# Kernel tuning notes

Measured on AMD Instinct MI355X. Metric: run time of the kernel, lower is better.

## Reference

```python
import jax, jax.numpy as jnp
import numpy as np


def setup_inputs() -> dict:
    key = jax.random.key(0)
    k1, k2 = jax.random.split(key)
    B, C, P, D, K = 8, 8, 512, 256, 8192
    z = jax.random.normal(k1, (B, C, P, D), dtype=jnp.float32)
    # codebook initialized with std = 1/sqrt(dim), matching nn.init.normal_
    codebook = jax.random.normal(k2, (K, D), dtype=jnp.float32) / np.sqrt(D).astype(np.float32)
    return {"z": z, "codebook": codebook}


def reference(z, codebook):
    B, C, P, D = z.shape
    z_flat = z.reshape(-1, D)  # [N, D]
    # squared-L2 distances: ||z||^2 - 2 z.cb^T + ||cb||^2  -> [N, K]
    dist = (
        jnp.sum(z_flat * z_flat, axis=1, keepdims=True)
        - 2.0 * jnp.matmul(z_flat, codebook.T)
        + jnp.sum(codebook * codebook, axis=1)[None, :]
    )
    codes = jnp.argmin(dist, axis=1)  # [N]
    z_q = codebook[codes].reshape(B, C, P, D)
    commit_loss = 0.25 * jnp.mean((jax.lax.stop_gradient(z_q) - z) ** 2)
    codebook_loss = jnp.mean((z_q - jax.lax.stop_gradient(z)) ** 2)
    total_loss = commit_loss + 0.25 * codebook_loss
    # straight-through estimator
    z_q_st = z + jax.lax.stop_gradient(z_q - z)
    return (z_q_st, total_loss, codes)
```

## Files before the change

### kernel.cpp

```cpp
#include <hip/hip_runtime.h>
#include <hip/hip_fp16.h>
#include <float.h>

typedef _Float16 half8 __attribute__((ext_vector_type(8)));
typedef _Float16 half4 __attribute__((ext_vector_type(4)));
typedef float floatx4 __attribute__((ext_vector_type(4)));

#define DD 256
#define D4 64
#define KK 8192
#define NROWS 32768
#define BM 64
#define BM2 32
#define BM4 128
#define NELEM 8388608
#define TAU1 2.5e-2f
#define TAU2 2e-3f
#define NSLICE 8
#define SLICE_K 1024
#define NBLOCKS2 1024
#define TILES_PER_BLOCK 4

#define WS_V9_BYTES      29360128
#define WS_CASCADE_BYTES 12582912
#define WS_R4_REFINE_BYTES 458768
#define WS_R4_FULL_BYTES   8849408

__global__ __launch_bounds__(256) void norms_kernel(
    const float* __restrict__ z, const float* __restrict__ cb,
    float* __restrict__ znorm, float* __restrict__ cbnorm)
{
    int wave = threadIdx.x >> 6;
    int lane = threadIdx.x & 63;
    int row = blockIdx.x * 4 + wave;
    const float4* src;
    float* dst;
    int r;
    if (row < NROWS) { src = (const float4*)z;  dst = znorm;  r = row; }
    else             { src = (const float4*)cb; dst = cbnorm; r = row - NROWS; }
    float4 v = src[(size_t)r * D4 + lane];
    float s = v.x*v.x + v.y*v.y + v.z*v.z + v.w*v.w;
    #pragma unroll
    for (int off = 1; off < 64; off <<= 1) s += __shfl_xor(s, off);
    if (lane == 0) dst[r] = s;
}

__global__ __launch_bounds__(256) void preconv_kernel(
    const float* __restrict__ cb, _Float16* __restrict__ bhi, _Float16* __restrict__ blo)
{
    size_t e4 = (size_t)blockIdx.x * 256 + threadIdx.x;
    float4 v = ((const float4*)cb)[e4];
    float t0 = v.x * 16.f, t1 = v.y * 16.f, t2 = v.z * 16.f, t3 = v.w * 16.f;
    _Float16 h0 = (_Float16)t0, h1 = (_Float16)t1, h2 = (_Float16)t2, h3 = (_Float16)t3;
    _Float16 l0 = (_Float16)((t0 - (float)h0) * 2048.f);
    _Float16 l1 = (_Float16)((t1 - (float)h1) * 2048.f);
    _Float16 l2 = (_Float16)((t2 - (float)h2) * 2048.f);
    _Float16 l3 = (_Float16)((t3 - (float)h3) * 2048.f);
    reinterpret_cast<half4*>(bhi)[e4] = half4{h0, h1, h2, h3};
    reinterpret_cast<half4*>(blo)[e4] = half4{l0, l1, l2, l3};
}

__global__ __launch_bounds__(256) void preconv_z_kernel(
    const float* __restrict__ z, _Float16* __restrict__ zg)
{
    int gid = blockIdx.x * 256 + threadIdx.x;
    int row = gid >> 5;
    int g   = gid & 31;
    int r   = row & 63;
    const float4* src = (const float4*)z + (size_t)row * D4 + g * 2;
    float4 a = src[0], b = src[1];
    half8 h = { (_Float16)a.x, (_Float16)a.y, (_Float16)a.z, (_Float16)a.w,
                (_Float16)b.x, (_Float16)b.y, (_Float16)b.z, (_Float16)b.w };
    int gp = g ^ (r & 7);
    *reinterpret_cast<half8*>((char*)zg + (size_t)(row >> 6) * 32768 + r * 512 + gp * 16) = h;
}

__global__ __launch_bounds__(256, 4) void vq_fp16_v11(
    const _Float16* __restrict__ zg,
    const _Float16* __restrict__ bhip, const float* __restrict__ cbnorm,
    float* __restrict__ pd, float* __restrict__ ps, int* __restrict__ pk)
{
    __shared__ _Float16 zt[BM * DD];

    const int tid  = threadIdx.x;
    const int lane = tid & 63;
    const int cg   = tid >> 6;
    const int l15  = lane & 15;
    const int lhi  = lane >> 4;
    const int slice = blockIdx.x & 7;
    const int grp   = blockIdx.x >> 3;

    const int A0 = l15 * 512 + ((lhi ^ (l15 & 3)) << 4) + (((l15 >> 2) & 1) << 6);
    int Ar[4];
    #pragma unroll
    for (int rf = 0; rf < 4; ++rf) Ar[rf] = A0 + rf * 8192;
    const char* zbase = (const char*)zt;

    const half8* bp = (const half8*)bhip + ((size_t)(slice * SLICE_K + cg * 32 + l15) * 32 + lhi);
    const float* cnp = cbnorm + slice * SLICE_K + cg * 32 + l15;
    const int kbase = slice * SLICE_K + cg * 32 + l15;

    #pragma unroll 1
    for (int j = 0; j < TILES_PER_BLOCK; ++j) {
        const int tileIdx = grp * TILES_PER_BLOCK + j;
        const int rowBase = tileIdx * BM;

        __syncthreads();
        {
            const float4* src = (const float4*)((const char*)zg + (size_t)tileIdx * 32768);
            float4* dst = (float4*)zt;
            #pragma unroll
            for (int i = 0; i < 8; ++i) dst[i * 256 + tid] = src[i * 256 + tid];
        }

        float bestd[4][4], secd[4][4];
        int   bestk[4][4];
        #pragma unroll
        for (int rf = 0; rf < 4; ++rf)
            #pragma unroll
            for (int reg = 0; reg < 4; ++reg) {
                bestd[rf][reg] = FLT_MAX; secd[rf][reg] = FLT_MAX; bestk[rf][reg] = 0;
            }

        __syncthreads();

        #pragma unroll 1
        for (int kt = 0; kt < SLICE_K / 128; ++kt) {
            floatx4 acc[4][2];
            #pragma unroll
            for (int rf = 0; rf < 4; ++rf)
                #pragma unroll
                for (int cf = 0; cf < 2; ++cf)
                    acc[rf][cf] = floatx4{0.f, 0.f, 0.f, 0.f};

            const half8* b0 = bp + kt * 4096;
            const half8* b1 = b0 + 512;

            #pragma unroll 2
            for (int dc = 0; dc < 8; ++dc) {
                half8 f0 = b0[dc * 4];
                half8 f1 = b1[dc * 4];
                #pragma unroll
                for (int rf = 0; rf < 4; ++rf) {
                    half8 a = *reinterpret_cast<const half8*>(zbase + (Ar[rf] ^ (dc << 6)));
                    acc[rf][0] = __builtin_amdgcn_mfma_f32_16x16x32_f16(a, f0, acc[rf][0], 0, 0, 0);
                    acc[rf][1] = __builtin_amdgcn_mfma_f32_16x16x32_f16(a, f1, acc[rf][1], 0, 0, 0);
                }
            }

            const float cn0 = cnp[kt * 128];
            const float cn1 = cnp[kt * 128 + 16];
            const int k0 = kbase + kt * 128;
            #pragma unroll
            for (int cf = 0; cf < 2; ++cf) {
                const float cn = cf ? cn1 : cn0;
                const int k = k0 + cf * 16;
                #pragma unroll
                for (int rf = 0; rf < 4; ++rf)
                    #pragma unroll
                    for (int reg = 0; reg < 4; ++reg) {
                        float m = fmaf(-0.125f, acc[rf][cf][reg], cn);
                        float w = fmaxf(bestd[rf][reg], m);
                        secd[rf][reg] = fminf(secd[rf][reg], w);
                        if (m < bestd[rf][reg]) { bestd[rf][reg] = m; bestk[rf][reg] = k; }
                    }
            }
        }

        #pragma unroll
        for (int off = 1; off < 16; off <<= 1) {
            #pragma unroll
            for (int rf = 0; rf < 4; ++rf)
                #pragma unroll
                for (int reg = 0; reg < 4; ++reg) {
                    float od = __shfl_xor(bestd[rf][reg], off);
                    int   ok = __shfl_xor(bestk[rf][reg], off);
                    float os = __shfl_xor(secd[rf][reg], off);
                    float hi = fmaxf(bestd[rf][reg], od);
                    secd[rf][reg] = fminf(fminf(secd[rf][reg], os), hi);
                    if (od < bestd[rf][reg] || (od == bestd[rf][reg] && ok < bestk[rf][reg])) {
                        bestd[rf][reg] = od; bestk[rf][reg] = ok;
                    }
                }
        }

        __syncthreads();
        float* dsc = reinterpret_cast<float*>(zt);
        int*   ksc = reinterpret_cast<int*>(zt) + 256;
        float* ssc = reinterpret_cast<float*>(zt) + 512;
        if (l15 == 0) {
            #pragma unroll
            for (int rf = 0; rf < 4; ++rf)
                #pragma unroll
                for (int reg = 0; reg < 4; ++reg) {
                    int rrow = rf * 16 + lhi * 4 + reg;
                    dsc[cg * 64 + rrow] = bestd[rf][reg];
                    ksc[cg * 64 + rrow] = bestk[rf][reg];
                    ssc[cg * 64 + rrow] = secd[rf][reg];
                }
        }
        __syncthreads();
        if (tid < 64) {
            float bd = dsc[tid];
            int   bk = ksc[tid];
            float sd = ssc[tid];
            #pragma unroll
            for (int c = 1; c < 4; ++c) {
                float od = dsc[c * 64 + tid];
                int   ok = ksc[c * 64 + tid];
                float os = ssc[c * 64 + tid];
                float hi = fmaxf(bd, od);
                sd = fminf(fminf(sd, os), hi);
                if (od < bd || (od == bd && ok < bk)) { bd = od; bk = ok; }
            }
            int row = rowBase + tid;
            pd[row * NSLICE + slice] = bd;
            ps[row * NSLICE + slice] = sd;
            pk[row * NSLICE + slice] = bk;
        }
    }
}

__global__ __launch_bounds__(256, 4) void vq_fp16_kernel(
    const float* __restrict__ z,
    const _Float16* __restrict__ bhip, const float* __restrict__ cbnorm,
    float* __restrict__ pd, float* __restrict__ ps, int* __restrict__ pk)
{
    __shared__ _Float16 zhi[BM * DD];
    const int tid  = threadIdx.x;
    const int lane = tid & 63;
    const int cg   = tid >> 6;
    const int l15  = lane & 15;
    const int lhi  = lane >> 4;
    const int slice = blockIdx.x & 7;
    const int grp   = blockIdx.x >> 3;
    const int sliceBase = slice * SLICE_K;

    int rowA[4];
    #pragma unroll
    for (int rf = 0; rf < 4; ++rf) rowA[rf] = rf * 16 + l15;

    #pragma unroll 1
    for (int j = 0; j < TILES_PER_BLOCK; ++j) {
        const int rowBase = (grp * TILES_PER_BLOCK + j) * BM;
        __syncthreads();
        #pragma unroll
        for (int i = 0; i < 16; ++i) {
            int gid = i * 256 + tid;
            int r   = gid >> 6;
            int c4  = gid & 63;
            float4 v = ((const float4*)z)[(size_t)(rowBase + r) * D4 + c4];
            _Float16 h0 = (_Float16)v.x, h1 = (_Float16)v.y,
                     h2 = (_Float16)v.z, h3 = (_Float16)v.w;
            int g = c4 >> 1;
            int byteOff = r * 512 + ((g ^ (r & 7)) << 4) + ((c4 & 1) << 3);
            *reinterpret_cast<half4*>(reinterpret_cast<char*>(zhi) + byteOff) = half4{h0, h1, h2, h3};
        }
        float bestd[4][4], secd[4][4];
        int   bestk[4][4];
        #pragma unroll
        for (int rf = 0; rf < 4; ++rf)
            #pragma unroll
            for (int reg = 0; reg < 4; ++reg) {
                bestd[rf][reg] = FLT_MAX; secd[rf][reg] = FLT_MAX; bestk[rf][reg] = 0;
            }
        __syncthreads();
        #pragma unroll 1
        for (int kt = 0; kt < SLICE_K / 128; ++kt) {
            floatx4 acc[4][2];
            #pragma unroll
            for (int rf = 0; rf < 4; ++rf)
                #pragma unroll
                for (int cf = 0; cf < 2; ++cf)
                    acc[rf][cf] = floatx4{0.f, 0.f, 0.f, 0.f};
            const int codeBase = sliceBase + kt * 128 + cg * 32 + l15;
            #pragma unroll 2
            for (int dc = 0; dc < 8; ++dc) {
                half8 bhi_f[2];
                #pragma unroll
                for (int cf = 0; cf < 2; ++cf) {
                    size_t off = (size_t)(codeBase + 16 * cf) * DD + dc * 32 + lhi * 8;
                    bhi_f[cf] = *reinterpret_cast<const half8*>(bhip + off);
                }
                #pragma unroll
                for (int rf = 0; rf < 4; ++rf) {
                    int g = dc * 4 + lhi;
                    int off = rowA[rf] * 512 + ((g ^ (rowA[rf] & 7)) << 4);
                    half8 ahi = *reinterpret_cast<const half8*>(reinterpret_cast<const char*>(zhi) + off);
                    #pragma unroll
                    for (int cf = 0; cf < 2; ++cf)
                        acc[rf][cf] = __builtin_amdgcn_mfma_f32_16x16x32_f16(ahi, bhi_f[cf], acc[rf][cf], 0, 0, 0);
                }
            }
            #pragma unroll
            for (int cf = 0; cf < 2; ++cf) {
                int k = codeBase + 16 * cf;
                float cn = cbnorm[k];
                #pragma unroll
                for (int rf = 0; rf < 4; ++rf)
                    #pragma unroll
                    for (int reg = 0; reg < 4; ++reg) {
                        float m = fmaf(-0.125f, acc[rf][cf][reg], cn);
                        float w = fmaxf(bestd[rf][reg], m);
                        secd[rf][reg] = fminf(secd[rf][reg], w);
                        if (m < bestd[rf][reg]) { bestd[rf][reg] = m; bestk[rf][reg] = k; }
                    }
            }
        }
        #pragma unroll
        for (int off = 1; off < 16; off <<= 1) {
            #pragma unroll
            for (int rf = 0; rf < 4; ++rf)
                #pragma unroll
                for (int reg = 0; reg < 4; ++reg) {
                    float od = __shfl_xor(bestd[rf][reg], off);
                    int   ok = __shfl_xor(bestk[rf][reg], off);
                    float os = __shfl_xor(secd[rf][reg], off);
                    float hi = fmaxf(bestd[rf][reg], od);
                    secd[rf][reg] = fminf(fminf(secd[rf][reg], os), hi);
                    if (od < bestd[rf][reg] || (od == bestd[rf][reg] && ok < bestk[rf][reg])) {
                        bestd[rf][reg] = od; bestk[rf][reg] = ok;
                    }
                }
        }
        __syncthreads();
        float* dsc = reinterpret_cast<float*>(zhi);
        int*   ksc = reinterpret_cast<int*>(zhi) + 256;
        float* ssc = reinterpret_cast<float*>(zhi) + 512;
        if (l15 == 0) {
            #pragma unroll
            for (int rf = 0; rf < 4; ++rf)
                #pragma unroll
                for (int reg = 0; reg < 4; ++reg) {
                    int rrow = rf * 16 + lhi * 4 + reg;
                    dsc[cg * 64 + rrow] = bestd[rf][reg];
                    ksc[cg * 64 + rrow] = bestk[rf][reg];
                    ssc[cg * 64 + rrow] = secd[rf][reg];
                }
        }
        __syncthreads();
        if (tid < 64) {
            float bd = dsc[tid];
            int   bk = ksc[tid];
            float sd = ssc[tid];
            #pragma unroll
            for (int c = 1; c < 4; ++c) {
                float od = dsc[c * 64 + tid];
                int   ok = ksc[c * 64 + tid];
                float os = ssc[c * 64 + tid];
                float hi = fmaxf(bd, od);
                sd = fminf(fminf(sd, os), hi);
                if (od < bd || (od == bd && ok < bk)) { bd = od; bk = ok; }
            }
            int row = rowBase + tid;
            pd[row * NSLICE + slice] = bd;
            ps[row * NSLICE + slice] = sd;
            pk[row * NSLICE + slice] = bk;
        }
    }
}

__global__ __launch_bounds__(256) void slice_reduce_kernel(
    const float* __restrict__ pd, const float* __restrict__ ps, const int* __restrict__ pk,
    int* __restrict__ codes, float* __restrict__ codes_f,
    int* __restrict__ cnt, int* __restrict__ list, float tau)
{
    int row = blockIdx.x * 256 + threadIdx.x;
    float bd = FLT_MAX, sd = FLT_MAX;
    int bk = 0;
    #pragma unroll
    for (int s = 0; s < NSLICE; ++s) {
        float d  = pd[row * NSLICE + s];
        int   k  = pk[row * NSLICE + s];
        float s2 = ps[row * NSLICE + s];
        float hi = fmaxf(bd, d);
        sd = fminf(fminf(sd, s2), hi);
        if (d < bd || (d == bd && k < bk)) { bd = d; bk = k; }
    }
    codes[row]   = bk;
    codes_f[row] = (float)bk;
    if ((sd - bd) < tau) {
        int idx = atomicAdd(cnt, 1);
        list[idx] = row;
    }
}

__global__ __launch_bounds__(256, 4) void vq_refine2_kernel(
    const float* __restrict__ z,
    const _Float16* __restrict__ bhip, const _Float16* __restrict__ blop,
    const float* __restrict__ cbnorm,
    const int* __restrict__ cnt, const int* __restrict__ list,
    float* __restrict__ pd, float* __restrict__ ps, int* __restrict__ pk)
{
    __shared__ _Float16 zhi[BM2 * DD];
    __shared__ _Float16 zlo[BM2 * DD];

    const int n1 = *cnt;
    if (n1 == 0) return;
    const int ntiles = (n1 + BM2 - 1) / BM2;
    const int njobs = ntiles * NSLICE;

    const int tid  = threadIdx.x;
    const int lane = tid & 63;
    const int cg   = tid >> 6;
    const int l15  = lane & 15;
    const int lhi  = lane >> 4;

    int rowA[2];
    #pragma unroll
    for (int rf = 0; rf < 2; ++rf) rowA[rf] = rf * 16 + l15;

    for (int job = blockIdx.x; job < njobs; job += gridDim.x) {
        const int slice = job & 7;
        const int tile  = job >> 3;
        const int base  = tile * BM2;
        const int sliceBase = slice * SLICE_K;

        __syncthreads();
        #pragma unroll
        for (int i = 0; i < 8; ++i) {
            int gid = i * 256 + tid;
            int r   = gid >> 6;
            int c4  = gid & 63;
            int pos = base + r;
            int row = list[pos < n1 ? pos : (n1 - 1)];
            float4 v = ((const float4*)z)[(size_t)row * D4 + c4];
            _Float16 h0 = (_Float16)v.x, h1 = (_Float16)v.y,
                     h2 = (_Float16)v.z, h3 = (_Float16)v.w;
            _Float16 e0 = (_Float16)((v.x - (float)h0) * 2048.f);
            _Float16 e1 = (_Float16)((v.y - (float)h1) * 2048.f);
            _Float16 e2 = (_Float16)((v.z - (float)h2) * 2048.f);
            _Float16 e3 = (_Float16)((v.w - (float)h3) * 2048.f);
            int g = c4 >> 1;
            int byteOff = r * 512 + ((g ^ (r & 7)) << 4) + ((c4 & 1) << 3);
            *reinterpret_cast<half4*>(reinterpret_cast<char*>(zhi) + byteOff) = half4{h0, h1, h2, h3};
            *reinterpret_cast<half4*>(reinterpret_cast<char*>(zlo) + byteOff) = half4{e0, e1, e2, e3};
        }

        float bestd[2][4], secd[2][4];
        int   bestk[2][4];
        #pragma unroll
        for (int rf = 0; rf < 2; ++rf)
            #pragma unroll
            for (int reg = 0; reg < 4; ++reg) {
                bestd[rf][reg] = FLT_MAX; secd[rf][reg] = FLT_MAX; bestk[rf][reg] = 0;
            }

        __syncthreads();

        #pragma unroll 1
        for (int kt = 0; kt < SLICE_K / 128; ++kt) {
            floatx4 accH[2][2], accM[2][2];
            #pragma unroll
            for (int rf = 0; rf < 2; ++rf)
                #pragma unroll
                for (int cf = 0; cf < 2; ++cf) {
                    accH[rf][cf] = floatx4{0.f, 0.f, 0.f, 0.f};
                    accM[rf][cf] = floatx4{0.f, 0.f, 0.f, 0.f};
                }
            const int codeBase = sliceBase + kt * 128 + cg * 32 + l15;
            #pragma unroll 2
            for (int dc = 0; dc < 8; ++dc) {
                half8 bhi_f[2], blo_f[2];
                #pragma unroll
                for (int cf = 0; cf < 2; ++cf) {
                    size_t off = (size_t)(codeBase + 16 * cf) * DD + dc * 32 + lhi * 8;
                    bhi_f[cf] = *reinterpret_cast<const half8*>(bhip + off);
                    blo_f[cf] = *reinterpret_cast<const half8*>(blop + off);
                }
                #pragma unroll
                for (int rf = 0; rf < 2; ++rf) {
                    int g = dc * 4 + lhi;
                    int off = rowA[rf] * 512 + ((g ^ (rowA[rf] & 7)) << 4);
                    half8 ahi = *reinterpret_cast<const half8*>(reinterpret_cast<const char*>(zhi) + off);
                    half8 alo = *reinterpret_cast<const half8*>(reinterpret_cast<const char*>(zlo) + off);
                    #pragma unroll
                    for (int cf = 0; cf < 2; ++cf) {
                        accH[rf][cf] = __builtin_amdgcn_mfma_f32_16x16x32_f16(ahi, bhi_f[cf], accH[rf][cf], 0, 0, 0);
                        accM[rf][cf] = __builtin_amdgcn_mfma_f32_16x16x32_f16(alo, bhi_f[cf], accM[rf][cf], 0, 0, 0);
                        accM[rf][cf] = __builtin_amdgcn_mfma_f32_16x16x32_f16(ahi, blo_f[cf], accM[rf][cf], 0, 0, 0);
                    }
                }
            }
            #pragma unroll
            for (int cf = 0; cf < 2; ++cf) {
                int k = codeBase + 16 * cf;
                float cn = cbnorm[k];
                #pragma unroll
                for (int rf = 0; rf < 2; ++rf)
                    #pragma unroll
                    for (int reg = 0; reg < 4; ++reg) {
                        float dot16 = fmaf(accM[rf][cf][reg], 0x1p-11f, accH[rf][cf][reg]);
                        float m = fmaf(-0.125f, dot16, cn);
                        float w = fmaxf(bestd[rf][reg], m);
                        secd[rf][reg] = fminf(secd[rf][reg], w);
                        if (m < bestd[rf][reg]) { bestd[rf][reg] = m; bestk[rf][reg] = k; }
                    }
            }
        }

        #pragma unroll
        for (int off = 1; off < 16; off <<= 1) {
            #pragma unroll
            for (int rf = 0; rf < 2; ++rf)
                #pragma unroll
                for (int reg = 0; reg < 4; ++reg) {
                    float od = __shfl_xor(bestd[rf][reg], off);
                    int   ok = __shfl_xor(bestk[rf][reg], off);
                    float os = __shfl_xor(secd[rf][reg], off);
                    float hi = fmaxf(bestd[rf][reg], od);
                    secd[rf][reg] = fminf(fminf(secd[rf][reg], os), hi);
                    if (od < bestd[rf][reg] || (od == bestd[rf][reg] && ok < bestk[rf][reg])) {
                        bestd[rf][reg] = od; bestk[rf][reg] = ok;
                    }
                }
        }

        __syncthreads();
        float* dsc = reinterpret_cast<float*>(zhi);
        int*   ksc = reinterpret_cast<int*>(zhi) + 128;
        float* ssc = reinterpret_cast<float*>(zhi) + 256;
        if (l15 == 0) {
            #pragma unroll
            for (int rf = 0; rf < 2; ++rf)
                #pragma unroll
                for (int reg = 0; reg < 4; ++reg) {
                    int rrow = rf * 16 + lhi * 4 + reg;
                    dsc[cg * 32 + rrow] = bestd[rf][reg];
                    ksc[cg * 32 + rrow] = bestk[rf][reg];
                    ssc[cg * 32 + rrow] = secd[rf][reg];
                }
        }
        __syncthreads();
        if (tid < 32) {
            float bd = dsc[tid];
            int   bk = ksc[tid];
            float sd = ssc[tid];
            #pragma unroll
            for (int c = 1; c < 4; ++c) {
                float od = dsc[c * 32 + tid];
                int   ok = ksc[c * 32 + tid];
                float os = ssc[c * 32 + tid];
                float hi = fmaxf(bd, od);
                sd = fminf(fminf(sd, os), hi);
                if (od < bd || (od == bd && ok < bk)) { bd = od; bk = ok; }
            }
            int pos = base + tid;
            pd[pos * NSLICE + slice] = bd;
            ps[pos * NSLICE + slice] = sd;
            pk[pos * NSLICE + slice] = bk;
        }
    }
}

__global__ __launch_bounds__(256) void slice_reduce2_kernel(
    const float* __restrict__ pd, const float* __restrict__ ps, const int* __restrict__ pk,
    const int* __restrict__ cnt, const int* __restrict__ list,
    int* __restrict__ codes, float* __restrict__ codes_f,
    int* __restrict__ cnt2, int* __restrict__ list2)
{
    const int n1 = *cnt;
    for (int i = blockIdx.x * 256 + threadIdx.x; i < n1; i += gridDim.x * 256) {
        float bd = FLT_MAX, sd = FLT_MAX;
        int bk = 0;
        #pragma unroll
        for (int s = 0; s < NSLICE; ++s) {
            float d  = pd[i * NSLICE + s];
            int   k  = pk[i * NSLICE + s];
            float s2 = ps[i * NSLICE + s];
            float hi = fmaxf(bd, d);
            sd = fminf(fminf(sd, s2), hi);
            if (d < bd || (d == bd && k < bk)) { bd = d; bk = k; }
        }
        int row = list[i];
        codes[row]   = bk;
        codes_f[row] = (float)bk;
        if ((sd - bd) < TAU2) {
            int idx = atomicAdd(cnt2, 1);
            list2[idx] = row;
        }
    }
}

__global__ __launch_bounds__(256) void refine_kernel(
    const float* __restrict__ z, const float* __restrict__ cb,
    const float* __restrict__ znorm, const float* __restrict__ cbnorm,
    const int* __restrict__ cnt, const int* __restrict__ list,
    int* __restrict__ codes, float* __restrict__ codes_f)
{
    __shared__ float zrow[DD];
    __shared__ float dred[4];
    __shared__ int   kred[4];
    const int tid = threadIdx.x;
    const int lane = tid & 63;
    const int wv = tid >> 6;
    const int n = *cnt;
    for (int i = blockIdx.x; i < n; i += gridDim.x) {
        const int row = list[i];
        if (tid < 64) ((float4*)zrow)[tid] = ((const float4*)z)[(size_t)row * D4 + tid];
        const float zn = znorm[row];
        __syncthreads();
        float bd = FLT_MAX;
        int   bk = 0;
        for (int k = tid; k < KK; k += 256) {
            const float4* crow = (const float4*)cb + (size_t)k * D4;
            float acc = 0.f;
            #pragma unroll 8
            for (int d4 = 0; d4 < D4; ++d4) {
                float4 c = crow[d4];
                float4 zv = ((const float4*)zrow)[d4];
                acc = fmaf(zv.x, c.x, acc);
                acc = fmaf(zv.y, c.y, acc);
                acc = fmaf(zv.z, c.z, acc);
                acc = fmaf(zv.w, c.w, acc);
            }
            float dist = fmaf(-2.f, acc, zn) + cbnorm[k];
            if (dist < bd) { bd = dist; bk = k; }
        }
        #pragma unroll
        for (int off = 1; off < 64; off <<= 1) {
            float od = __shfl_xor(bd, off);
            int   ok = __shfl_xor(bk, off);
            if (od < bd || (od == bd && ok < bk)) { bd = od; bk = ok; }
        }
        if (lane == 0) { dred[wv] = bd; kred[wv] = bk; }
        __syncthreads();
        if (tid == 0) {
            #pragma unroll
            for (int c = 1; c < 4; ++c) {
                if (dred[c] < bd || (dred[c] == bd && kred[c] < bk)) { bd = dred[c]; bk = kred[c]; }
            }
            codes[row]   = bk;
            codes_f[row] = (float)bk;
        }
        __syncthreads();
    }
}

__global__ __launch_bounds__(256) void gather_loss_kernel(
    const float* __restrict__ z, const float* __restrict__ cb,
    const int* __restrict__ codes, float* __restrict__ zq_out,
    float* __restrict__ partials)
{
    __shared__ float red[4];
    int tid = threadIdx.x;
    size_t e4 = (size_t)blockIdx.x * 256 + tid;
    int row = (int)(e4 >> 6);
    int d4  = (int)(e4 & 63);
    int code = codes[row];
    float4 q  = ((const float4*)cb)[(size_t)code * D4 + d4];
    float4 zv = ((const float4*)z)[e4];
    float dx = q.x - zv.x, dy = q.y - zv.y, dz = q.z - zv.z, dw = q.w - zv.w;
    float4 o;
    o.x = zv.x + dx; o.y = zv.y + dy; o.z = zv.z + dz; o.w = zv.w + dw;
    ((float4*)zq_out)[e4] = o;
    float s = dx*dx + dy*dy + dz*dz + dw*dw;
    #pragma unroll
    for (int off = 1; off < 64; off <<= 1) s += __shfl_xor(s, off);
    if ((tid & 63) == 0) red[tid >> 6] = s;
    __syncthreads();
    if (tid == 0) partials[blockIdx.x] = ((red[0] + red[1]) + red[2]) + red[3];
}

__global__ __launch_bounds__(256) void final_loss_kernel(
    const float* __restrict__ partials, float* __restrict__ out_loss)
{
    __shared__ float red[4];
    int tid = threadIdx.x;
    float s = 0.f;
    #pragma unroll 4
    for (int i = 0; i < 32; ++i) s += partials[tid * 32 + i];
    #pragma unroll
    for (int off = 1; off < 64; off <<= 1) s += __shfl_xor(s, off);
    if ((tid & 63) == 0) red[tid >> 6] = s;
    __syncthreads();
    if (tid == 0) {
        float tot = ((red[0] + red[1]) + red[2]) + red[3];
        out_loss[0] = 0.5f * (tot / (float)NELEM);
    }
}

template <bool PRECONV, bool REFINE>
__global__ __launch_bounds__(512, 1) void vq_mfma_kernel(
    const float* __restrict__ z, const float* __restrict__ cb,
    const _Float16* __restrict__ bhip, const _Float16* __restrict__ blop,
    const float* __restrict__ znorm, const float* __restrict__ cbnorm,
    int* __restrict__ codes, float* __restrict__ codes_f,
    int* __restrict__ cnt, int* __restrict__ list)
{
    __shared__ _Float16 zhi[BM4 * DD];
    __shared__ _Float16 zlo[BM4 * DD];
    const int tid  = threadIdx.x;
    const int lane = tid & 63;
    const int w    = tid >> 6;
    const int rg   = w >> 2;
    const int cg   = w & 3;
    const int l15  = lane & 15;
    const int lhi  = lane >> 4;
    const int rowBase = blockIdx.x * BM4;

    #pragma unroll
    for (int i = 0; i < 16; ++i) {
        int gid = i * 512 + tid;
        int r   = gid >> 6;
        int c4  = gid & 63;
        float4 v = ((const float4*)z)[(size_t)(rowBase + r) * D4 + c4];
        _Float16 h0 = (_Float16)v.x, h1 = (_Float16)v.y,
                 h2 = (_Float16)v.z, h3 = (_Float16)v.w;
        _Float16 e0 = (_Float16)((v.x - (float)h0) * 2048.f);
        _Float16 e1 = (_Float16)((v.y - (float)h1) * 2048.f);
        _Float16 e2 = (_Float16)((v.z - (float)h2) * 2048.f);
        _Float16 e3 = (_Float16)((v.w - (float)h3) * 2048.f);
        int g = c4 >> 1;
        int byteOff = r * 512 + (((g ^ (r & 7))) << 4) + ((c4 & 1) << 3);
        *reinterpret_cast<half4*>(reinterpret_cast<char*>(zhi) + byteOff) = half4{h0, h1, h2, h3};
        *reinterpret_cast<half4*>(reinterpret_cast<char*>(zlo) + byteOff) = half4{e0, e1, e2, e3};
    }
    int rowA[4];
    #pragma unroll
    for (int rf = 0; rf < 4; ++rf) rowA[rf] = rg * 64 + rf * 16 + l15;
    float zn[4][4];
    #pragma unroll
    for (int rf = 0; rf < 4; ++rf)
        #pragma unroll
        for (int reg = 0; reg < 4; ++reg)
            zn[rf][reg] = znorm[rowBase + rg * 64 + rf * 16 + lhi * 4 + reg];
    float bestd[4][4], secd[4][4];
    int   bestk[4][4];
    #pragma unroll
    for (int rf = 0; rf < 4; ++rf)
        #pragma unroll
        for (int reg = 0; reg < 4; ++reg) {
            bestd[rf][reg] = FLT_MAX; secd[rf][reg] = FLT_MAX; bestk[rf][reg] = 0;
        }
    __syncthreads();
    for (int kt = 0; kt < KK / 256; ++kt) {
        floatx4 accH[4][4], accM[4][4];
        #pragma unroll
        for (int rf = 0; rf < 4; ++rf)
            #pragma unroll
            for (int cf = 0; cf < 4; ++cf) {
                accH[rf][cf] = floatx4{0.f, 0.f, 0.f, 0.f};
                accM[rf][cf] = floatx4{0.f, 0.f, 0.f, 0.f};
            }
        const int codeBase = kt * 256 + cg * 64 + l15;
        for (int dc = 0; dc < 8; ++dc) {
            half8 bhi_f[4], blo_f[4];
            #pragma unroll
            for (int cf = 0; cf < 4; ++cf) {
                if (PRECONV) {
                    size_t off = (size_t)(codeBase + 16 * cf) * DD + dc * 32 + lhi * 8;
                    bhi_f[cf] = *reinterpret_cast<const half8*>(bhip + off);
                    blo_f[cf] = *reinterpret_cast<const half8*>(blop + off);
                } else {
                    const float4* p = (const float4*)(cb + (size_t)(codeBase + 16 * cf) * DD + dc * 32 + lhi * 8);
                    float4 u0 = p[0];
                    float4 u1 = p[1];
                    float uv[8] = {u0.x, u0.y, u0.z, u0.w, u1.x, u1.y, u1.z, u1.w};
                    half8 bh, bl;
                    #pragma unroll
                    for (int jj = 0; jj < 8; ++jj) {
                        float t = uv[jj] * 16.f;
                        _Float16 h = (_Float16)t;
                        bh[jj] = h;
                        bl[jj] = (_Float16)((t - (float)h) * 2048.f);
                    }
                    bhi_f[cf] = bh; blo_f[cf] = bl;
                }
            }
            #pragma unroll
            for (int rf = 0; rf < 4; ++rf) {
                int g = dc * 4 + lhi;
                int off = rowA[rf] * 512 + ((g ^ (rowA[rf] & 7)) << 4);
                half8 ahi = *reinterpret_cast<const half8*>(reinterpret_cast<const char*>(zhi) + off);
                half8 alo = *reinterpret_cast<const half8*>(reinterpret_cast<const char*>(zlo) + off);
                #pragma unroll
                for (int cf = 0; cf < 4; ++cf) {
                    accH[rf][cf] = __builtin_amdgcn_mfma_f32_16x16x32_f16(ahi, bhi_f[cf], accH[rf][cf], 0, 0, 0);
                    accM[rf][cf] = __builtin_amdgcn_mfma_f32_16x16x32_f16(alo, bhi_f[cf], accM[rf][cf], 0, 0, 0);
                    accM[rf][cf] = __builtin_amdgcn_mfma_f32_16x16x32_f16(ahi, blo_f[cf], accM[rf][cf], 0, 0, 0);
                }
            }
        }
        #pragma unroll
        for (int cf = 0; cf < 4; ++cf) {
            int k = codeBase + 16 * cf;
            float cn = cbnorm[k];
            #pragma unroll
            for (int rf = 0; rf < 4; ++rf)
                #pragma unroll
                for (int reg = 0; reg < 4; ++reg) {
                    float dot16 = fmaf(accM[rf][cf][reg], 0x1p-11f, accH[rf][cf][reg]);
                    float dist  = fmaf(-0.125f, dot16, zn[rf][reg]) + cn;
                    float wv2 = fmaxf(bestd[rf][reg], dist);
                    secd[rf][reg] = fminf(secd[rf][reg], wv2);
                    if (dist < bestd[rf][reg]) { bestd[rf][reg] = dist; bestk[rf][reg] = k; }
                }
        }
    }
    #pragma unroll
    for (int off = 1; off < 16; off <<= 1) {
        #pragma unroll
        for (int rf = 0; rf < 4; ++rf)
            #pragma unroll
            for (int reg = 0; reg < 4; ++reg) {
                float od = __shfl_xor(bestd[rf][reg], off);
                int   ok = __shfl_xor(bestk[rf][reg], off);
                float os = __shfl_xor(secd[rf][reg], off);
                float hi = fmaxf(bestd[rf][reg], od);
                secd[rf][reg] = fminf(fminf(secd[rf][reg], os), hi);
                if (od < bestd[rf][reg] || (od == bestd[rf][reg] && ok < bestk[rf][reg])) {
                    bestd[rf][reg] = od; bestk[rf][reg] = ok;
                }
            }
    }
    __syncthreads();
    float* dsc = reinterpret_cast<float*>(zhi);
    int*   ksc = reinterpret_cast<int*>(zhi) + 512;
    float* ssc = reinterpret_cast<float*>(zhi) + 1024;
    if (l15 == 0) {
        #pragma unroll
        for (int rf = 0; rf < 4; ++rf)
            #pragma unroll
            for (int reg = 0; reg < 4; ++reg) {
                int rrow = rg * 64 + rf * 16 + lhi * 4 + reg;
                dsc[cg * 128 + rrow] = bestd[rf][reg];
                ksc[cg * 128 + rrow] = bestk[rf][reg];
                ssc[cg * 128 + rrow] = secd[rf][reg];
            }
    }
    __syncthreads();
    if (tid < 128) {
        float bd = dsc[tid];
        int   bk = ksc[tid];
        float sd = ssc[tid];
        #pragma unroll
        for (int c = 1; c < 4; ++c) {
            float od = dsc[c * 128 + tid];
            int   ok = ksc[c * 128 + tid];
            float os = ssc[c * 128 + tid];
            float hi = fmaxf(bd, od);
            sd = fminf(fminf(sd, os), hi);
            if (od < bd || (od == bd && ok < bk)) { bd = od; bk = ok; }
        }
        int row = rowBase + tid;
        codes[row]   = bk;
        codes_f[row] = (float)bk;
        if (REFINE && (sd - bd) < TAU2) {
            int idx = atomicAdd(cnt, 1);
            list[idx] = row;
        }
    }
}

extern "C" void kernel_launch(void* const* d_in, const int* in_sizes, int n_in,
                              void* d_out, int out_size, void* d_ws, size_t ws_size,
                              hipStream_t stream) {
    const float* z  = (const float*)d_in[0];
    const float* cb = (const float*)d_in[1];
    float* out      = (float*)d_out;
    float* zq_out   = out;
    float* loss_out = out + NELEM;
    float* codes_f  = out + NELEM + 1;

    char* wsb       = (char*)d_ws;
    float* znorm    = (float*)(wsb + 0);
    float* cbnorm   = (float*)(wsb + 131072);
    int*   codes    = (int*)(wsb + 163840);
    float* partials = (float*)(wsb + 294912);
    int*   cnt      = (int*)(wsb + 327680);
    int*   cnt2     = (int*)(wsb + 327684);
    int*   list     = (int*)(wsb + 327696);

    norms_kernel<<<10240, 256, 0, stream>>>(z, cb, znorm, cbnorm);

    if (ws_size >= (size_t)WS_CASCADE_BYTES) {
        int*   list2  = (int*)(wsb + 460800);
        float* pd     = (float*)(wsb + 593920);
        float* ps     = (float*)(wsb + 1642496);
        int*   pk     = (int*)(wsb + 2691072);
        _Float16* bhi = (_Float16*)(wsb + 4194304);
        _Float16* blo = (_Float16*)(wsb + 8388608);
        hipMemsetAsync(cnt, 0, 8, stream);
        preconv_kernel<<<2048, 256, 0, stream>>>(cb, bhi, blo);
        if (ws_size >= (size_t)WS_V9_BYTES) {
            _Float16* zg = (_Float16*)(wsb + 12582912);
            preconv_z_kernel<<<4096, 256, 0, stream>>>(z, zg);
            vq_fp16_v11<<<NBLOCKS2, 256, 0, stream>>>(zg, bhi, cbnorm, pd, ps, pk);
        } else {
            vq_fp16_kernel<<<NBLOCKS2, 256, 0, stream>>>(z, bhi, cbnorm, pd, ps, pk);
        }
        slice_reduce_kernel<<<128, 256, 0, stream>>>(pd, ps, pk, codes, codes_f, cnt, list, TAU1);
        vq_refine2_kernel<<<512, 256, 0, stream>>>(z, bhi, blo, cbnorm, cnt, list, pd, ps, pk);
        slice_reduce2_kernel<<<64, 256, 0, stream>>>(pd, ps, pk, cnt, list, codes, codes_f, cnt2, list2);
        refine_kernel<<<256, 256, 0, stream>>>(z, cb, znorm, cbnorm, cnt2, list2, codes, codes_f);
    } else {
        _Float16* bhi = (_Float16*)(wsb + 460800);
        _Float16* blo = (_Float16*)(wsb + 4655104);
        const bool preconv = ws_size >= (size_t)WS_R4_FULL_BYTES;
        const bool refine  = ws_size >= (size_t)WS_R4_REFINE_BYTES;
        if (refine) hipMemsetAsync(cnt, 0, sizeof(int), stream);
        if (preconv) preconv_kernel<<<2048, 256, 0, stream>>>(cb, bhi, blo);
        if (preconv && refine)
            vq_mfma_kernel<true, true><<<NROWS / BM4, 512, 0, stream>>>(z, cb, bhi, blo, znorm, cbnorm, codes, codes_f, cnt, list);
        else if (preconv)
            vq_mfma_kernel<true, false><<<NROWS / BM4, 512, 0, stream>>>(z, cb, bhi, blo, znorm, cbnorm, codes, codes_f, cnt, list);
        else if (refine)
            vq_mfma_kernel<false, true><<<NROWS / BM4, 512, 0, stream>>>(z, cb, bhi, blo, znorm, cbnorm, codes, codes_f, cnt, list);
        else
            vq_mfma_kernel<false, false><<<NROWS / BM4, 512, 0, stream>>>(z, cb, bhi, blo, znorm, cbnorm, codes, codes_f, cnt, list);
        if (refine)
            refine_kernel<<<256, 256, 0, stream>>>(z, cb, znorm, cbnorm, cnt, list, codes, codes_f);
    }

    gather_loss_kernel<<<8192, 256, 0, stream>>>(z, cb, codes, zq_out, partials);
    final_loss_kernel<<<1, 256, 0, stream>>>(partials, loss_out);
}
```

Before: 624.0 us.

## Halve first-stage tolerance, split refine stage into finer slices, fuse z norms

```diff
diff --git a/kernel.cpp b/kernel.cpp
--- a/kernel.cpp
+++ b/kernel.cpp
@@ -14,15 +14,18 @@
 #define BM2 32
 #define BM4 128
 #define NELEM 8388608
-#define TAU1 2.5e-2f
+#define TAU1 1.25e-2f
 #define TAU2 2e-3f
 #define NSLICE 8
 #define SLICE_K 1024
-#define NBLOCKS2 1024
+#define NVS 16
+#define VS_K 512
+#define NBLOCKS1 1024
 #define TILES_PER_BLOCK 4
 
 #define WS_V9_BYTES      29360128
 #define WS_CASCADE_BYTES 12582912
+#define WS_SLICED2_BYTES 7800832
 #define WS_R4_REFINE_BYTES 458768
 #define WS_R4_FULL_BYTES   8849408
 
@@ -45,6 +48,19 @@
     if (lane == 0) dst[r] = s;
 }
 
+__global__ __launch_bounds__(256) void cbnorm_kernel(
+    const float* __restrict__ cb, float* __restrict__ cbnorm)
+{
+    int wave = threadIdx.x >> 6;
+    int lane = threadIdx.x & 63;
+    int r = blockIdx.x * 4 + wave;
+    float4 v = ((const float4*)cb)[(size_t)r * D4 + lane];
+    float s = v.x*v.x + v.y*v.y + v.z*v.z + v.w*v.w;
+    #pragma unroll
+    for (int off = 1; off < 64; off <<= 1) s += __shfl_xor(s, off);
+    if (lane == 0) cbnorm[r] = s;
+}
+
 __global__ __launch_bounds__(256) void preconv_kernel(
     const float* __restrict__ cb, _Float16* __restrict__ bhi, _Float16* __restrict__ blo)
 {
@@ -61,7 +77,7 @@
 }
 
 __global__ __launch_bounds__(256) void preconv_z_kernel(
-    const float* __restrict__ z, _Float16* __restrict__ zg)
+    const float* __restrict__ z, _Float16* __restrict__ zg, float* __restrict__ znorm)
 {
     int gid = blockIdx.x * 256 + threadIdx.x;
     int row = gid >> 5;
@@ -73,6 +89,11 @@
                 (_Float16)b.x, (_Float16)b.y, (_Float16)b.z, (_Float16)b.w };
     int gp = g ^ (r & 7);
     *reinterpret_cast<half8*>((char*)zg + (size_t)(row >> 6) * 32768 + r * 512 + gp * 16) = h;
+    float s = a.x*a.x + a.y*a.y + a.z*a.z + a.w*a.w
+            + b.x*b.x + b.y*b.y + b.z*b.z + b.w*b.w;
+    #pragma unroll
+    for (int off = 1; off < 32; off <<= 1) s += __shfl_xor(s, off);
+    if ((threadIdx.x & 31) == 0) znorm[row] = s;
 }
 
 __global__ __launch_bounds__(256, 4) void vq_fp16_v11(
@@ -390,7 +411,7 @@
     const _Float16* __restrict__ bhip, const _Float16* __restrict__ blop,
     const float* __restrict__ cbnorm,
     const int* __restrict__ cnt, const int* __restrict__ list,
-    float* __restrict__ pd, float* __restrict__ ps, int* __restrict__ pk)
+    float* __restrict__ pd2, float* __restrict__ ps2, int* __restrict__ pk2)
 {
     __shared__ _Float16 zhi[BM2 * DD];
     __shared__ _Float16 zlo[BM2 * DD];
@@ -398,7 +419,7 @@
     const int n1 = *cnt;
     if (n1 == 0) return;
     const int ntiles = (n1 + BM2 - 1) / BM2;
-    const int njobs = ntiles * NSLICE;
+    const int njobs = ntiles * NVS;
 
     const int tid  = threadIdx.x;
     const int lane = tid & 63;
@@ -411,10 +432,10 @@
     for (int rf = 0; rf < 2; ++rf) rowA[rf] = rf * 16 + l15;
 
     for (int job = blockIdx.x; job < njobs; job += gridDim.x) {
-        const int slice = job & 7;
-        const int tile  = job >> 3;
+        const int vs    = job & (NVS - 1);
+        const int tile  = job >> 4;
         const int base  = tile * BM2;
-        const int sliceBase = slice * SLICE_K;
+        const int vsBase = vs * VS_K;
 
         __syncthreads();
         #pragma unroll
@@ -449,7 +470,7 @@
         __syncthreads();
 
         #pragma unroll 1
-        for (int kt = 0; kt < SLICE_K / 128; ++kt) {
+        for (int kt = 0; kt < VS_K / 128; ++kt) {
             floatx4 accH[2][2], accM[2][2];
             #pragma unroll
             for (int rf = 0; rf < 2; ++rf)
@@ -458,7 +479,7 @@
                     accH[rf][cf] = floatx4{0.f, 0.f, 0.f, 0.f};
                     accM[rf][cf] = floatx4{0.f, 0.f, 0.f, 0.f};
                 }
-            const int codeBase = sliceBase + kt * 128 + cg * 32 + l15;
+            const int codeBase = vsBase + kt * 128 + cg * 32 + l15;
             #pragma unroll 2
             for (int dc = 0; dc < 8; ++dc) {
                 half8 bhi_f[2], blo_f[2];
@@ -546,15 +567,15 @@
                 if (od < bd || (od == bd && ok < bk)) { bd = od; bk = ok; }
             }
             int pos = base + tid;
-            pd[pos * NSLICE + slice] = bd;
-            ps[pos * NSLICE + slice] = sd;
-            pk[pos * NSLICE + slice] = bk;
+            pd2[pos * NVS + vs] = bd;
+            ps2[pos * NVS + vs] = sd;
+            pk2[pos * NVS + vs] = bk;
         }
     }
 }
 
 __global__ __launch_bounds__(256) void slice_reduce2_kernel(
-    const float* __restrict__ pd, const float* __restrict__ ps, const int* __restrict__ pk,
+    const float* __restrict__ pd2, const float* __restrict__ ps2, const int* __restrict__ pk2,
     const int* __restrict__ cnt, const int* __restrict__ list,
     int* __restrict__ codes, float* __restrict__ codes_f,
     int* __restrict__ cnt2, int* __restrict__ list2)
@@ -564,10 +585,10 @@
         float bd = FLT_MAX, sd = FLT_MAX;
         int bk = 0;
         #pragma unroll
-        for (int s = 0; s < NSLICE; ++s) {
-            float d  = pd[i * NSLICE + s];
-            int   k  = pk[i * NSLICE + s];
-            float s2 = ps[i * NSLICE + s];
+        for (int s = 0; s < NVS; ++s) {
+            float d  = pd2[i * NVS + s];
+            int   k  = pk2[i * NVS + s];
+            float s2 = ps2[i * NVS + s];
             float hi = fmaxf(bd, d);
             sd = fminf(fminf(sd, s2), hi);
             if (d < bd || (d == bd && k < bk)) { bd = d; bk = k; }
@@ -872,9 +893,28 @@
     int*   cnt2     = (int*)(wsb + 327684);
     int*   list     = (int*)(wsb + 327696);
 
-    norms_kernel<<<10240, 256, 0, stream>>>(z, cb, znorm, cbnorm);
-
-    if (ws_size >= (size_t)WS_CASCADE_BYTES) {
+    if (ws_size >= (size_t)WS_V9_BYTES) {
+        int*   list2  = (int*)(wsb + 460800);
+        float* pd     = (float*)(wsb + 593920);
+        float* ps     = (float*)(wsb + 1642496);
+        int*   pk     = (int*)(wsb + 2691072);
+        _Float16* bhi = (_Float16*)(wsb + 4194304);
+        _Float16* blo = (_Float16*)(wsb + 8388608);
+        _Float16* zg  = (_Float16*)(wsb + 12582912);
+        float* pd2    = (float*)(wsb + 12582912);
+        float* ps2    = (float*)(wsb + 12582912 + 2097152);
+        int*   pk2    = (int*)(wsb + 12582912 + 4194304);
+
+        hipMemsetAsync(cnt, 0, 8, stream);
+        cbnorm_kernel<<<2048, 256, 0, stream>>>(cb, cbnorm);
+        preconv_kernel<<<2048, 256, 0, stream>>>(cb, bhi, blo);
+        preconv_z_kernel<<<4096, 256, 0, stream>>>(z, zg, znorm);
+        vq_fp16_v11<<<NBLOCKS1, 256, 0, stream>>>(zg, bhi, cbnorm, pd, ps, pk);
+        slice_reduce_kernel<<<128, 256, 0, stream>>>(pd, ps, pk, codes, codes_f, cnt, list, TAU1);
+        vq_refine2_kernel<<<512, 256, 0, stream>>>(z, bhi, blo, cbnorm, cnt, list, pd2, ps2, pk2);
+        slice_reduce2_kernel<<<64, 256, 0, stream>>>(pd2, ps2, pk2, cnt, list, codes, codes_f, cnt2, list2);
+        refine_kernel<<<256, 256, 0, stream>>>(z, cb, znorm, cbnorm, cnt2, list2, codes, codes_f);
+    } else if (ws_size >= (size_t)WS_CASCADE_BYTES) {
         int*   list2  = (int*)(wsb + 460800);
         float* pd     = (float*)(wsb + 593920);
         float* ps     = (float*)(wsb + 1642496);
@@ -882,23 +922,17 @@
         _Float16* bhi = (_Float16*)(wsb + 4194304);
         _Float16* blo = (_Float16*)(wsb + 8388608);
         hipMemsetAsync(cnt, 0, 8, stream);
+        norms_kernel<<<10240, 256, 0, stream>>>(z, cb, znorm, cbnorm);
         preconv_kernel<<<2048, 256, 0, stream>>>(cb, bhi, blo);
-        if (ws_size >= (size_t)WS_V9_BYTES) {
-            _Float16* zg = (_Float16*)(wsb + 12582912);
-            preconv_z_kernel<<<4096, 256, 0, stream>>>(z, zg);
-            vq_fp16_v11<<<NBLOCKS2, 256, 0, stream>>>(zg, bhi, cbnorm, pd, ps, pk);
-        } else {
-            vq_fp16_kernel<<<NBLOCKS2, 256, 0, stream>>>(z, bhi, cbnorm, pd, ps, pk);
-        }
+        vq_fp16_kernel<<<NBLOCKS1, 256, 0, stream>>>(z, bhi, cbnorm, pd, ps, pk);
         slice_reduce_kernel<<<128, 256, 0, stream>>>(pd, ps, pk, codes, codes_f, cnt, list, TAU1);
-        vq_refine2_kernel<<<512, 256, 0, stream>>>(z, bhi, blo, cbnorm, cnt, list, pd, ps, pk);
-        slice_reduce2_kernel<<<64, 256, 0, stream>>>(pd, ps, pk, cnt, list, codes, codes_f, cnt2, list2);
-        refine_kernel<<<256, 256, 0, stream>>>(z, cb, znorm, cbnorm, cnt2, list2, codes, codes_f);
+        refine_kernel<<<256, 256, 0, stream>>>(z, cb, znorm, cbnorm, cnt, list, codes, codes_f);
     } else {
         _Float16* bhi = (_Float16*)(wsb + 460800);
         _Float16* blo = (_Float16*)(wsb + 4655104);
         const bool preconv = ws_size >= (size_t)WS_R4_FULL_BYTES;
         const bool refine  = ws_size >= (size_t)WS_R4_REFINE_BYTES;
+        norms_kernel<<<10240, 256, 0, stream>>>(z, cb, znorm, cbnorm);
         if (refine) hipMemsetAsync(cnt, 0, sizeof(int), stream);
         if (preconv) preconv_kernel<<<2048, 256, 0, stream>>>(cb, bhi, blo);
         if (preconv && refine)
```

Result: faster. 595.1 us (-4.6%).
